# Performance work log

Measured on AMD Instinct MI355X. Metric: run time of the kernel, lower is better.

The kernel has to match this reference:

```python
import jax, jax.numpy as jnp
import numpy as np
from jax import lax

B, DEPTH, FS, C, NH = 4, 160, 4, 96, 4  # batch, temporal depth, feature_size, model_dims, heads
N = DEPTH * FS * FS                      # 2560 tokens
HD = C // NH                             # head dim 24
THETA = 0.6
BN_EPS = 1e-5
DN = ('NCDHW', 'OIDHW', 'NCDHW')


def setup_inputs() -> dict:
    key = jax.random.key(0)
    ks = jax.random.split(key, 16)
    x = jax.random.normal(ks[0], (B, N, C), jnp.float32)
    wq = jax.random.normal(ks[1], (C, C, 3, 3, 3), jnp.float32) * 0.02
    wk = jax.random.normal(ks[2], (C, C, 3, 3, 3), jnp.float32) * 0.02
    wv = jax.random.normal(ks[3], (C, C, 1, 1, 1), jnp.float32) * 0.1
    wo = jax.random.normal(ks[4], (C, C), jnp.float32) * 0.05
    bo = jnp.zeros((C,), jnp.float32)
    bnq_gamma = 1.0 + 0.1 * jax.random.normal(ks[5], (C,), jnp.float32)
    bnq_beta = 0.1 * jax.random.normal(ks[6], (C,), jnp.float32)
    bnq_mean = 0.1 * jax.random.normal(ks[7], (C,), jnp.float32)
    bnq_var = jax.random.uniform(ks[8], (C,), jnp.float32) + 0.5
    bnk_gamma = 1.0 + 0.1 * jax.random.normal(ks[9], (C,), jnp.float32)
    bnk_beta = 0.1 * jax.random.normal(ks[10], (C,), jnp.float32)
    bnk_mean = 0.1 * jax.random.normal(ks[11], (C,), jnp.float32)
    bnk_var = jax.random.uniform(ks[12], (C,), jnp.float32) + 0.5
    sharp_gradient = jnp.float32(np.sqrt(HD))
    return dict(x=x, sharp_gradient=sharp_gradient,
                wq=wq, bnq_gamma=bnq_gamma, bnq_beta=bnq_beta, bnq_mean=bnq_mean, bnq_var=bnq_var,
                wk=wk, bnk_gamma=bnk_gamma, bnk_beta=bnk_beta, bnk_mean=bnk_mean, bnk_var=bnk_var,
                wv=wv, wo=wo, bo=bo)


def _conv3d(x, w, pad):
    return lax.conv_general_dilated(x, w, (1, 1, 1), [(pad, pad)] * 3, dimension_numbers=DN)


def _tcdc(x, w):
    # normal conv + temporal center-difference correction
    out_normal = _conv3d(x, w, 1)
    kernel_diff = (w[:, :, 0].sum((-1, -2)) + w[:, :, -1].sum((-1, -2)))[:, :, None, None, None]
    out_diff = _conv3d(x, kernel_diff, 0)
    return out_normal - THETA * out_diff


def _bn(x, gamma, beta, mean, var):
    # eval-mode BatchNorm3d over channel axis 1
    sh = (1, -1, 1, 1, 1)
    scale = gamma.reshape(sh) * lax.rsqrt(var.reshape(sh) + BN_EPS)
    return (x - mean.reshape(sh)) * scale + beta.reshape(sh)


def _to_heads(t):
    # (B,C,D,H,W) -> (B,NH,N,HD)
    b = t.shape[0]
    t = t.reshape(b, C, N).transpose(0, 2, 1)          # (B,N,C)
    return t.reshape(b, N, NH, HD).transpose(0, 2, 1, 3)


def reference(x, sharp_gradient, wq, bnq_gamma, bnq_beta, bnq_mean, bnq_var,
              wk, bnk_gamma, bnk_beta, bnk_mean, bnk_var, wv, wo, bo):
    b = x.shape[0]
    xv = x.transpose(0, 2, 1).reshape(b, C, DEPTH, FS, FS)  # (B,C,D,H,W)
    q = _bn(_tcdc(xv, wq), bnq_gamma, bnq_beta, bnq_mean, bnq_var)
    k = _bn(_tcdc(xv, wk), bnk_gamma, bnk_beta, bnk_mean, bnk_var)
    v = _conv3d(xv, wv, 0)
    q, k, v = _to_heads(q), _to_heads(k), _to_heads(v)
    scores = jnp.einsum('bhnd,bhmd->bhnm', q, k) / sharp_gradient
    attn = jax.nn.softmax(scores, axis=-1)
    out = jnp.einsum('bhnm,bhmd->bhnd', attn, v)
    out = out.transpose(0, 2, 1, 3).reshape(b, N, C)   # merge heads
    return out @ wo.T + bo                              # out projection (dropout=eval)
```

## Files before the change

kernel.cpp:

```cpp
#include <hip/hip_runtime.h>
#include <hip/hip_bf16.h>

#define BB 4
#define DEPTH 160
#define CC 96
#define NN 2560
#define NHH 4
#define HD 24
#define THETA 0.6f
#define BN_EPS 1e-5f

typedef __attribute__((ext_vector_type(4))) float f32x4;
typedef __attribute__((ext_vector_type(8))) short s16x8;
typedef __attribute__((ext_vector_type(4))) short s16x4;
typedef __attribute__((ext_vector_type(2))) unsigned u32x2;
typedef __attribute__((ext_vector_type(4))) unsigned u32x4;

#if __has_builtin(__builtin_amdgcn_exp2f)
#define EXP2(x) __builtin_amdgcn_exp2f(x)
#else
#define EXP2(x) exp2f(x)
#endif

#define WS_WQ   0
#define WS_WK   124416
#define WS_WV   248832
#define WS_BQ   253440
#define WS_BK   253536
#define WS_ATT  253632
#define WS_QB   1236672
#define WS_KB   1892032
#define WS_VT   2547392
#define WS_WO   3202752

__device__ __forceinline__ short f2bf(float f) {
    unsigned u = __float_as_uint(f);
    u += 0x7fffu + ((u >> 16) & 1u);
    return (short)(u >> 16);
}
__device__ __forceinline__ unsigned bf16pk(float lo, float hi) {
    unsigned r;
    asm("v_cvt_pk_bf16_f32 %0, %1, %2" : "=v"(r) : "v"(lo), "v"(hi));
    return r;
}
__device__ __forceinline__ int vslot(int n) {
    return (n & 32) | (((n >> 2) & 3) << 3) | (((n >> 4) & 1) << 2) | (n & 3);
}

__global__ void prep_w(const float* __restrict__ w, const float* __restrict__ gamma,
                       const float* __restrict__ beta, const float* __restrict__ mean,
                       const float* __restrict__ var, short* __restrict__ w_eff,
                       float* __restrict__ bias,
                       const float* __restrict__ wv, short* __restrict__ wv_b) {
    int oc = blockIdx.x;
    int ic = threadIdx.x;
    if (ic >= CC) return;
    float scale = gamma[oc] * rsqrtf(var[oc] + BN_EPS);
    if (ic == 0) bias[oc] = beta[oc] - mean[oc] * scale;
    const float* wp = w + (oc * CC + ic) * 27;
    float kdiff = 0.f;
#pragma unroll
    for (int t = 0; t < 9; ++t) kdiff += wp[t] + wp[18 + t];
#pragma unroll
    for (int t = 0; t < 27; ++t) {
        float v = wp[t];
        if (t == 13) v -= THETA * kdiff;
        w_eff[t * (CC * CC) + oc * CC + ic] = f2bf(v * scale);
    }
    if (wv_b) wv_b[oc * CC + ic] = f2bf(wv[oc * CC + ic]);
}

__global__ void prep_wo(const float* __restrict__ wo, short* __restrict__ wo_b) {
    int i = blockIdx.x * 256 + threadIdx.x;
    if (i < CC * CC) {
        int oc = i / CC, ic = i % CC;
        wo_b[(((oc >> 4) * 3 + (ic >> 5)) << 9) + (oc & 15) * 32 + (ic & 31)] = f2bf(wo[i]);
    }
}

__global__ __launch_bounds__(192) void qkv_conv(
        const float* __restrict__ x, const short* __restrict__ wq_b,
        const short* __restrict__ wk_b, const short* __restrict__ wv_b,
        const float* __restrict__ bias_q, const float* __restrict__ bias_k,
        const float* __restrict__ sgp,
        short* __restrict__ Qb, short* __restrict__ Kb, short* __restrict__ Vtp) {
    __shared__ __align__(16) short xs[65 * 104];
    const int b = blockIdx.y;
    const int d0 = blockIdx.x * 2;
    const int z = blockIdx.z;
    const int tid = threadIdx.x;

#pragma unroll
    for (int k = 0; k < 8; ++k) {
        int c = tid + k * 192;
        int row = c / 24, ic0 = (c % 24) * 4;
        int dg = d0 - 1 + (row >> 4), pos = row & 15;
        u32x2 o = {0u, 0u};
        if (dg >= 0 && dg < DEPTH) {
            f32x4 v = *(const f32x4*)(x + ((size_t)(b * NN + dg * 16 + pos)) * CC + ic0);
            o[0] = bf16pk(v[0], v[1]);
            o[1] = bf16pk(v[2], v[3]);
        }
        *(u32x2*)&xs[row * 104 + ic0] = o;
    }
    if (tid < 26) *(u32x2*)&xs[64 * 104 + tid * 4] = (u32x2){0u, 0u};
    __syncthreads();

    const int w  = tid >> 6, l = tid & 63;
    const int j  = l & 15, g = l >> 4;
    const int oc0 = z * 48 + w * 16;
    const int hj = j >> 2, wj = j & 3;

    const short* wqlane = wq_b + (oc0 + j) * CC + 8 * g;
    const short* wklane = wk_b + (oc0 + j) * CC + 8 * g;
    const short* wvlane = wv_b + (oc0 + j) * CC + 8 * g;

    f32x4 accQA = {0,0,0,0}, accQB = {0,0,0,0};
    f32x4 accKA = {0,0,0,0}, accKB = {0,0,0,0};
    f32x4 avA   = {0,0,0,0}, avB   = {0,0,0,0};

    s16x8 wqc[3], wkc[3], wqn[3], wkn[3];
#pragma unroll
    for (int icb = 0; icb < 3; ++icb) {
        wqc[icb] = *(const s16x8*)(wqlane + icb * 32);
        wkc[icb] = *(const s16x8*)(wklane + icb * 32);
    }

#pragma unroll
    for (int tap = 0; tap < 27; ++tap) {
        if (tap < 26) {
#pragma unroll
            for (int icb = 0; icb < 3; ++icb) {
                wqn[icb] = *(const s16x8*)(wqlane + (tap + 1) * (CC * CC) + icb * 32);
                wkn[icb] = *(const s16x8*)(wklane + (tap + 1) * (CC * CC) + icb * 32);
            }
        }
        const int kd = tap / 9, kh = (tap / 3) % 3, kw = tap % 3;
        const int hh = hj + kh - 1, ww = wj + kw - 1;
        const bool valid = ((unsigned)hh < 4u) && ((unsigned)ww < 4u);
        const int rA = valid ? (kd * 16 + hh * 4 + ww) : 64;
        const int rB = valid ? ((1 + kd) * 16 + hh * 4 + ww) : 64;
        const short* xrA = &xs[rA * 104 + 8 * g];
        const short* xrB = &xs[rB * 104 + 8 * g];
#pragma unroll
        for (int icb = 0; icb < 3; ++icb) {
            s16x8 afA = *(const s16x8*)(xrA + icb * 32);
            s16x8 afB = *(const s16x8*)(xrB + icb * 32);
            accQA = __builtin_amdgcn_mfma_f32_16x16x32_bf16(afA, wqc[icb], accQA, 0, 0, 0);
            accQB = __builtin_amdgcn_mfma_f32_16x16x32_bf16(afB, wqc[icb], accQB, 0, 0, 0);
            accKA = __builtin_amdgcn_mfma_f32_16x16x32_bf16(afA, wkc[icb], accKA, 0, 0, 0);
            accKB = __builtin_amdgcn_mfma_f32_16x16x32_bf16(afB, wkc[icb], accKB, 0, 0, 0);
            if (tap == 13) {
                s16x8 bv = *(const s16x8*)(wvlane + icb * 32);
                avA = __builtin_amdgcn_mfma_f32_16x16x32_bf16(afA, bv, avA, 0, 0, 0);
                avB = __builtin_amdgcn_mfma_f32_16x16x32_bf16(afB, bv, avB, 0, 0, 0);
            }
        }
        if (tap < 26) {
#pragma unroll
            for (int icb = 0; icb < 3; ++icb) {
                wqc[icb] = wqn[icb];
                wkc[icb] = wkn[icb];
            }
        }
    }

    const float qs = 1.4426950408889634f / sgp[0];
    const int oc = oc0 + j, h = oc / HD, hd = oc % HD;
    const float bq_ = bias_q[oc], bk_ = bias_k[oc];
    const size_t headbase = (size_t)(b * NHH + h) * NN;
    short* QpA = Qb + (headbase + (d0 + 0) * 16 + 4 * g) * 32 + hd;
    short* QpB = Qb + (headbase + (d0 + 1) * 16 + 4 * g) * 32 + hd;
    short* KpA = Kb + (headbase + (d0 + 0) * 16 + 4 * g) * 32 + hd;
    short* KpB = Kb + (headbase + (d0 + 1) * 16 + 4 * g) * 32 + hd;
#pragma unroll
    for (int r = 0; r < 4; ++r) {
        QpA[r * 32] = f2bf((accQA[r] + bq_) * qs);
        QpB[r * 32] = f2bf((accQB[r] + bq_) * qs);
        KpA[r * 32] = f2bf(accKA[r] + bk_);
        KpB[r * 32] = f2bf(accKB[r] + bk_);
    }
    {
        short* Vb = Vtp + (size_t)(b * NHH + h) * (NN * 32);
        const int dh = hd >> 4, dj = hd & 15;
#pragma unroll
        for (int r = 0; r < 4; ++r) {
            int nA = d0 * 16 + 4 * g + r;
            int nB = nA + 16;
            int wA = vslot(nA & 63), wB = vslot(nB & 63);
            Vb[(nA >> 6) * 2048 + ((wA >> 5) * 2 + dh) * 512 + dj * 32 + (wA & 31)] = f2bf(avA[r]);
            Vb[(nB >> 6) * 2048 + ((wB >> 5) * 2 + dh) * 512 + dj * 32 + (wB & 31)] = f2bf(avB[r]);
        }
    }
    if (z == 0 && w == 0) {
        const int n = (d0 + ((l >> 4) & 1)) * 16 + (l & 15);
        const s16x8 z8 = {0, 0, 0, 0, 0, 0, 0, 0};
#pragma unroll
        for (int it = 0; it < 2; ++it) {
            int h2 = (l >> 5) + 2 * it;
            *(s16x8*)(Qb + ((size_t)(b * NHH + h2) * NN + n) * 32 + 24) = z8;
            *(s16x8*)(Kb + ((size_t)(b * NHH + h2) * NN + n) * 32 + 24) = z8;
        }
        const int wN = vslot(n & 63);
#pragma unroll
        for (int it2 = 0; it2 < 2; ++it2) {
            int h3 = it2 * 2 + (l >> 5);
            short* pb = Vtp + (size_t)(b * NHH + h3) * (NN * 32)
                      + (n >> 6) * 2048 + ((wN >> 5) * 2 + 1) * 512 + (wN & 31);
#pragma unroll
            for (int dj = 8; dj < 16; ++dj)
                pb[dj * 32] = 0;
        }
    }
}

#define SOFTTILE(S0, S1, S2, S3, MX, LP, OA, OB, P0, P1) {                      \
    float v0 = fmaxf(fmaxf(S0[0], S0[1]), fmaxf(S0[2], S0[3]));                 \
    float v1 = fmaxf(fmaxf(S1[0], S1[1]), fmaxf(S1[2], S1[3]));                 \
    float v2 = fmaxf(fmaxf(S2[0], S2[1]), fmaxf(S2[2], S2[3]));                 \
    float v3 = fmaxf(fmaxf(S3[0], S3[1]), fmaxf(S3[2], S3[3]));                 \
    float vmx = fmaxf(fmaxf(v0, v1), fmaxf(v2, v3));                            \
    vmx = fmaxf(vmx, __shfl_xor(vmx, 16));                                      \
    vmx = fmaxf(vmx, __shfl_xor(vmx, 32));                                      \
    float nm = fmaxf(MX, vmx);                                                  \
    float sc = EXP2(MX - nm);                                                   \
    MX = nm;                                                                    \
    LP *= sc; OA *= sc; OB *= sc;                                               \
    float p00 = EXP2(S0[0] - MX), p01 = EXP2(S0[1] - MX);                       \
    float p02 = EXP2(S0[2] - MX), p03 = EXP2(S0[3] - MX);                       \
    float p10 = EXP2(S1[0] - MX), p11 = EXP2(S1[1] - MX);                       \
    float p12 = EXP2(S1[2] - MX), p13 = EXP2(S1[3] - MX);                       \
    float p20 = EXP2(S2[0] - MX), p21 = EXP2(S2[1] - MX);                       \
    float p22 = EXP2(S2[2] - MX), p23 = EXP2(S2[3] - MX);                       \
    float p30 = EXP2(S3[0] - MX), p31 = EXP2(S3[1] - MX);                       \
    float p32 = EXP2(S3[2] - MX), p33 = EXP2(S3[3] - MX);                       \
    LP += (((p00 + p01) + (p02 + p03)) + ((p10 + p11) + (p12 + p13)))           \
        + (((p20 + p21) + (p22 + p23)) + ((p30 + p31) + (p32 + p33)));          \
    u32x4 w0_ = { bf16pk(p00, p01), bf16pk(p02, p03),                           \
                  bf16pk(p10, p11), bf16pk(p12, p13) };                         \
    u32x4 w1_ = { bf16pk(p20, p21), bf16pk(p22, p23),                           \
                  bf16pk(p30, p31), bf16pk(p32, p33) };                         \
    P0 = __builtin_bit_cast(s16x8, w0_);                                        \
    P1 = __builtin_bit_cast(s16x8, w1_);                                        \
}

__global__ __launch_bounds__(256) void attn_kernel(
        const short* __restrict__ Qb, const short* __restrict__ Kb,
        const short* __restrict__ Vtp, float* __restrict__ att) {
    __shared__ __align__(16) float comb[3][64][20];
    const int bh = blockIdx.x & 15;
    const int q0 = (blockIdx.x >> 4) * 32;
    const int b = bh >> 2, h = bh & 3;
    const int tid = threadIdx.x, wvid = tid >> 6, l = tid & 63;
    const int j = l & 15, g = l >> 4;

    const s16x8 qf0 = *(const s16x8*)(Qb + ((size_t)bh * NN + q0 + j) * 32 + 8 * g);
    const s16x8 qf1 = *(const s16x8*)(Qb + ((size_t)bh * NN + q0 + 16 + j) * 32 + 8 * g);
    const short* Kbase = Kb  + (size_t)bh * NN * 32 + (size_t)j * 32 + 8 * g;
    const short* Vbase = Vtp + (size_t)bh * NN * 32 + (size_t)j * 32 + 8 * g;

    f32x4 oA0 = {0,0,0,0}, oB0 = {0,0,0,0};
    f32x4 oA1 = {0,0,0,0}, oB1 = {0,0,0,0};
    float mx0 = -1e30f, lp0 = 0.f, mx1 = -1e30f, lp1 = 0.f;
    const f32x4 z = {0,0,0,0};

    const int tbeg = wvid * (NN / 4);
    const int tend = tbeg + NN / 4;

    for (int t0 = tbeg; t0 < tend; t0 += 64) {
        const short* kp = Kbase + (size_t)t0 * 32;
        s16x8 k0 = *(const s16x8*)(kp);
        s16x8 k1 = *(const s16x8*)(kp + 512);
        s16x8 k2 = *(const s16x8*)(kp + 1024);
        s16x8 k3 = *(const s16x8*)(kp + 1536);
        const short* vp = Vbase + (size_t)t0 * 32;
        s16x8 vA0 = *(const s16x8*)(vp);
        s16x8 vB0 = *(const s16x8*)(vp + 512);
        s16x8 vA1 = *(const s16x8*)(vp + 1024);
        s16x8 vB1 = *(const s16x8*)(vp + 1536);

        f32x4 s0 = __builtin_amdgcn_mfma_f32_16x16x32_bf16(k0, qf0, z, 0, 0, 0);
        f32x4 s1 = __builtin_amdgcn_mfma_f32_16x16x32_bf16(k1, qf0, z, 0, 0, 0);
        f32x4 s2 = __builtin_amdgcn_mfma_f32_16x16x32_bf16(k2, qf0, z, 0, 0, 0);
        f32x4 s3 = __builtin_amdgcn_mfma_f32_16x16x32_bf16(k3, qf0, z, 0, 0, 0);
        s16x8 P00, P01;
        SOFTTILE(s0, s1, s2, s3, mx0, lp0, oA0, oB0, P00, P01)

        f32x4 t0s = __builtin_amdgcn_mfma_f32_16x16x32_bf16(k0, qf1, z, 0, 0, 0);
        f32x4 t1s = __builtin_amdgcn_mfma_f32_16x16x32_bf16(k1, qf1, z, 0, 0, 0);
        f32x4 t2s = __builtin_amdgcn_mfma_f32_16x16x32_bf16(k2, qf1, z, 0, 0, 0);
        f32x4 t3s = __builtin_amdgcn_mfma_f32_16x16x32_bf16(k3, qf1, z, 0, 0, 0);
        s16x8 P10, P11;
        SOFTTILE(t0s, t1s, t2s, t3s, mx1, lp1, oA1, oB1, P10, P11)

        oA0 = __builtin_amdgcn_mfma_f32_16x16x32_bf16(vA0, P00, oA0, 0, 0, 0);
        oA0 = __builtin_amdgcn_mfma_f32_16x16x32_bf16(vA1, P01, oA0, 0, 0, 0);
        oB0 = __builtin_amdgcn_mfma_f32_16x16x32_bf16(vB0, P00, oB0, 0, 0, 0);
        oB0 = __builtin_amdgcn_mfma_f32_16x16x32_bf16(vB1, P01, oB0, 0, 0, 0);
        oA1 = __builtin_amdgcn_mfma_f32_16x16x32_bf16(vA0, P10, oA1, 0, 0, 0);
        oA1 = __builtin_amdgcn_mfma_f32_16x16x32_bf16(vA1, P11, oA1, 0, 0, 0);
        oB1 = __builtin_amdgcn_mfma_f32_16x16x32_bf16(vB0, P10, oB1, 0, 0, 0);
        oB1 = __builtin_amdgcn_mfma_f32_16x16x32_bf16(vB1, P11, oB1, 0, 0, 0);
    }

    lp0 += __shfl_xor(lp0, 16); lp0 += __shfl_xor(lp0, 32);
    lp1 += __shfl_xor(lp1, 16); lp1 += __shfl_xor(lp1, 32);

    if (wvid != 0) {
        float* cp = comb[wvid - 1][l];
        cp[0] = mx0; cp[1] = lp0; cp[2] = mx1; cp[3] = lp1;
        *(f32x4*)(cp + 4)  = oA0;
        *(f32x4*)(cp + 8)  = oB0;
        *(f32x4*)(cp + 12) = oA1;
        *(f32x4*)(cp + 16) = oB1;
    }
    __syncthreads();
    if (wvid != 0) return;

#pragma unroll
    for (int wv = 0; wv < 3; ++wv) {
        const float* cp = comb[wv][l];
        {
            float mb = cp[0], lb = cp[1];
            f32x4 oAb = *(const f32x4*)(cp + 4);
            f32x4 oBb = *(const f32x4*)(cp + 8);
            float mm = fmaxf(mx0, mb);
            float sa = EXP2(mx0 - mm), sb = EXP2(mb - mm);
            mx0 = mm;
            lp0 = lp0 * sa + lb * sb;
            oA0 = oA0 * sa + oAb * sb;
            oB0 = oB0 * sa + oBb * sb;
        }
        {
            float mb = cp[2], lb = cp[3];
            f32x4 oAb = *(const f32x4*)(cp + 12);
            f32x4 oBb = *(const f32x4*)(cp + 16);
            float mm = fmaxf(mx1, mb);
            float sa = EXP2(mx1 - mm), sb = EXP2(mb - mm);
            mx1 = mm;
            lp1 = lp1 * sa + lb * sb;
            oA1 = oA1 * sa + oAb * sb;
            oB1 = oB1 * sa + oBb * sb;
        }
    }

    const float rl0 = 1.f / lp0, rl1 = 1.f / lp1;
    f32x4 rA0 = oA0 * rl0, rB0 = oB0 * rl0;
    f32x4 rA1 = oA1 * rl1, rB1 = oB1 * rl1;

    float* op0 = att + ((size_t)b * NN + q0 + j) * CC + h * HD;
    float* op1 = att + ((size_t)b * NN + q0 + 16 + j) * CC + h * HD;
    *(f32x4*)(op0 + 4 * g) = rA0;
    *(f32x4*)(op1 + 4 * g) = rA1;
    if (g < 2) {
        *(f32x4*)(op0 + 16 + 4 * g) = rB0;
        *(f32x4*)(op1 + 16 + 4 * g) = rB1;
    }
}

__global__ __launch_bounds__(256) void proj_kernel(
        const float* __restrict__ att, const short* __restrict__ wo_b,
        const float* __restrict__ bo, float* __restrict__ out) {
    __shared__ __align__(16) short als[64 * 104];
    const int t0 = blockIdx.x * 64;
    const int tid = threadIdx.x;
#pragma unroll
    for (int k = 0; k < 6; ++k) {
        int c = tid + k * 256;
        int row = c / 24, ic0 = (c % 24) * 4;
        f32x4 v = *(const f32x4*)(att + (size_t)(t0 + row) * CC + ic0);
        u32x2 o = { bf16pk(v[0], v[1]), bf16pk(v[2], v[3]) };
        *(u32x2*)&als[row * 104 + ic0] = o;
    }
    __syncthreads();

    const int w = tid >> 6, l = tid & 63;
    const int j = l & 15, g = l >> 4;
    const short* ap = &als[(w * 16 + j) * 104 + 8 * g];
    s16x8 a0 = *(const s16x8*)(ap);
    s16x8 a1 = *(const s16x8*)(ap + 32);
    s16x8 a2 = *(const s16x8*)(ap + 64);
    const f32x4 zz = {0, 0, 0, 0};
    float* ob = out + (size_t)(t0 + w * 16 + 4 * g) * CC + j;
#pragma unroll
    for (int oct = 0; oct < 6; ++oct) {
        const short* wp = wo_b + oct * 3 * 512 + j * 32 + 8 * g;
        f32x4 acc = zz;
        acc = __builtin_amdgcn_mfma_f32_16x16x32_bf16(a0, *(const s16x8*)(wp),        acc, 0, 0, 0);
        acc = __builtin_amdgcn_mfma_f32_16x16x32_bf16(a1, *(const s16x8*)(wp + 512),  acc, 0, 0, 0);
        acc = __builtin_amdgcn_mfma_f32_16x16x32_bf16(a2, *(const s16x8*)(wp + 1024), acc, 0, 0, 0);
        const float bb = bo[oct * 16 + j];
#pragma unroll
        for (int r = 0; r < 4; ++r)
            ob[(size_t)r * CC + oct * 16] = acc[r] + bb;
    }
}

extern "C" void kernel_launch(void* const* d_in, const int* in_sizes, int n_in,
                              void* d_out, int out_size, void* d_ws, size_t ws_size,
                              hipStream_t stream) {
    const float* x     = (const float*)d_in[0];
    const float* sg    = (const float*)d_in[1];
    const float* wq    = (const float*)d_in[2];
    const float* bnq_g = (const float*)d_in[3];
    const float* bnq_b = (const float*)d_in[4];
    const float* bnq_m = (const float*)d_in[5];
    const float* bnq_v = (const float*)d_in[6];
    const float* wk    = (const float*)d_in[7];
    const float* bnk_g = (const float*)d_in[8];
    const float* bnk_b = (const float*)d_in[9];
    const float* bnk_m = (const float*)d_in[10];
    const float* bnk_v = (const float*)d_in[11];
    const float* wv    = (const float*)d_in[12];
    const float* wo    = (const float*)d_in[13];
    const float* bo    = (const float*)d_in[14];

    float* ws = (float*)d_ws;
    short* wq_b   = (short*)(ws + WS_WQ);
    short* wk_b   = (short*)(ws + WS_WK);
    short* wv_b   = (short*)(ws + WS_WV);
    float* bias_q = ws + WS_BQ;
    float* bias_k = ws + WS_BK;
    float* attw   = ws + WS_ATT;
    short* Qb     = (short*)(ws + WS_QB);
    short* Kb     = (short*)(ws + WS_KB);
    short* Vtp    = (short*)(ws + WS_VT);
    short* wo_b   = (short*)(ws + WS_WO);

    prep_w<<<dim3(CC), dim3(128), 0, stream>>>(wq, bnq_g, bnq_b, bnq_m, bnq_v, wq_b, bias_q,
                                               wv, wv_b);
    prep_w<<<dim3(CC), dim3(128), 0, stream>>>(wk, bnk_g, bnk_b, bnk_m, bnk_v, wk_b, bias_k,
                                               nullptr, nullptr);
    prep_wo<<<dim3(36), dim3(256), 0, stream>>>(wo, wo_b);

    qkv_conv<<<dim3(DEPTH / 2, BB, 2), dim3(192), 0, stream>>>(
        x, wq_b, wk_b, wv_b, bias_q, bias_k, sg, Qb, Kb, Vtp);

    attn_kernel<<<dim3(NN / 32 * 16), dim3(256), 0, stream>>>(Qb, Kb, Vtp, attw);

    proj_kernel<<<dim3(BB * NN / 64), dim3(256), 0, stream>>>(attw, wo_b, bo, (float*)d_out);
}
```

Baseline: 78.48 us.

## Stage conv weights through LDS in two-tap groups with fragment-major layout

The Q/K weight prep now writes weights in a fragment-major layout indexed by tap, output-channel half, 16-oc tile and 32-ic block. The conv kernel loads two taps of Q and K weights cooperatively into shared memory per group and reads MFMA B-fragments from LDS, replacing per-lane global loads with register double-buffering. This gives coalesced 16-byte global loads and shares weights across the three waves. In exchange it adds about 36 KB of LDS per block, two barriers per group and a non-unrolled outer loop, which may cut occupancy and serialize load and compute.

```diff
diff --git a/kernel.cpp b/kernel.cpp
--- a/kernel.cpp
+++ b/kernel.cpp
@@ -61,11 +61,14 @@
     float kdiff = 0.f;
 #pragma unroll
     for (int t = 0; t < 9; ++t) kdiff += wp[t] + wp[18 + t];
+    const int zh = oc / 48, oct = (oc % 48) >> 4, jj = oc & 15;
+    const int icb = ic >> 5, icw = ic & 31;
+    const int fo = oct * 3 + icb;
 #pragma unroll
     for (int t = 0; t < 27; ++t) {
         float v = wp[t];
         if (t == 13) v -= THETA * kdiff;
-        w_eff[t * (CC * CC) + oc * CC + ic] = f2bf(v * scale);
+        w_eff[(size_t)((t * 2 + zh) * 9 + fo) * 512 + jj * 32 + icw] = f2bf(v * scale);
     }
     if (wv_b) wv_b[oc * CC + ic] = f2bf(wv[oc * CC + ic]);
 }
@@ -85,6 +88,7 @@
         const float* __restrict__ sgp,
         short* __restrict__ Qb, short* __restrict__ Kb, short* __restrict__ Vtp) {
     __shared__ __align__(16) short xs[65 * 104];
+    __shared__ __align__(16) short wl[4 * 4608];
     const int b = blockIdx.y;
     const int d0 = blockIdx.x * 2;
     const int z = blockIdx.z;
@@ -104,63 +108,85 @@
         *(u32x2*)&xs[row * 104 + ic0] = o;
     }
     if (tid < 26) *(u32x2*)&xs[64 * 104 + tid * 4] = (u32x2){0u, 0u};
-    __syncthreads();
 
     const int w  = tid >> 6, l = tid & 63;
     const int j  = l & 15, g = l >> 4;
     const int oc0 = z * 48 + w * 16;
     const int hj = j >> 2, wj = j & 3;
-
-    const short* wqlane = wq_b + (oc0 + j) * CC + 8 * g;
-    const short* wklane = wk_b + (oc0 + j) * CC + 8 * g;
+    const int lof = j * 32 + 8 * g;
+
     const short* wvlane = wv_b + (oc0 + j) * CC + 8 * g;
+    s16x8 bv0 = *(const s16x8*)(wvlane);
+    s16x8 bv1 = *(const s16x8*)(wvlane + 32);
+    s16x8 bv2 = *(const s16x8*)(wvlane + 64);
 
     f32x4 accQA = {0,0,0,0}, accQB = {0,0,0,0};
     f32x4 accKA = {0,0,0,0}, accKB = {0,0,0,0};
     f32x4 avA   = {0,0,0,0}, avB   = {0,0,0,0};
 
-    s16x8 wqc[3], wkc[3], wqn[3], wkn[3];
-#pragma unroll
-    for (int icb = 0; icb < 3; ++icb) {
-        wqc[icb] = *(const s16x8*)(wqlane + icb * 32);
-        wkc[icb] = *(const s16x8*)(wklane + icb * 32);
-    }
-
-#pragma unroll
-    for (int tap = 0; tap < 27; ++tap) {
-        if (tap < 26) {
+    __syncthreads();
+
+#pragma unroll 1
+    for (int grp = 0; grp < 14; ++grp) {
+        const int g0 = grp * 2;
+        const int two = (g0 < 26) ? 1 : 0;
+        const int nchunk = two ? 12 : 6;
+        const int perarr = two ? 1152 : 576;
+        s16x8 tmp[12];
+        int dsts[12];
+#pragma unroll
+        for (int i = 0; i < 12; ++i) {
+            if (i < nchunk) {
+                int idx = tid + i * 192;
+                int arr = (idx >= perarr) ? 1 : 0;
+                int ridx = idx - arr * perarr;
+                int tp = (ridx >= 576) ? 1 : 0;
+                int rem = (ridx - tp * 576) * 8;
+                const short* gsrc = (arr ? wk_b : wq_b)
+                    + (size_t)((g0 + tp) * 2 + z) * 4608 + rem;
+                tmp[i] = *(const s16x8*)gsrc;
+                dsts[i] = (arr * 2 + tp) * 4608 + rem;
+            }
+        }
+        __syncthreads();
+#pragma unroll
+        for (int i = 0; i < 12; ++i)
+            if (i < nchunk) *(s16x8*)&wl[dsts[i]] = tmp[i];
+        __syncthreads();
+
+#pragma unroll
+        for (int tp = 0; tp < 2; ++tp) {
+            const int tap = g0 + tp;
+            if (tap > 26) break;
+            const int kd = tap / 9, kh = (tap / 3) % 3, kw = tap % 3;
+            const int hh = hj + kh - 1, ww = wj + kw - 1;
+            const bool valid = ((unsigned)hh < 4u) && ((unsigned)ww < 4u);
+            const int rA = valid ? (kd * 16 + hh * 4 + ww) : 64;
+            const int rB = valid ? ((1 + kd) * 16 + hh * 4 + ww) : 64;
+            const short* xrA = &xs[rA * 104 + 8 * g];
+            const short* xrB = &xs[rB * 104 + 8 * g];
+            const short* wqf = &wl[tp * 4608 + (w * 3) * 512 + lof];
+            const short* wkf = &wl[(2 + tp) * 4608 + (w * 3) * 512 + lof];
 #pragma unroll
             for (int icb = 0; icb < 3; ++icb) {
-                wqn[icb] = *(const s16x8*)(wqlane + (tap + 1) * (CC * CC) + icb * 32);
-                wkn[icb] = *(const s16x8*)(wklane + (tap + 1) * (CC * CC) + icb * 32);
+                s16x8 afA = *(const s16x8*)(xrA + icb * 32);
+                s16x8 afB = *(const s16x8*)(xrB + icb * 32);
+                s16x8 bq  = *(const s16x8*)(wqf + icb * 512);
+                s16x8 bk  = *(const s16x8*)(wkf + icb * 512);
+                accQA = __builtin_amdgcn_mfma_f32_16x16x32_bf16(afA, bq, accQA, 0, 0, 0);
+                accQB = __builtin_amdgcn_mfma_f32_16x16x32_bf16(afB, bq, accQB, 0, 0, 0);
+                accKA = __builtin_amdgcn_mfma_f32_16x16x32_bf16(afA, bk, accKA, 0, 0, 0);
+                accKB = __builtin_amdgcn_mfma_f32_16x16x32_bf16(afB, bk, accKB, 0, 0, 0);
             }
-        }
-        const int kd = tap / 9, kh = (tap / 3) % 3, kw = tap % 3;
-        const int hh = hj + kh - 1, ww = wj + kw - 1;
-        const bool valid = ((unsigned)hh < 4u) && ((unsigned)ww < 4u);
-        const int rA = valid ? (kd * 16 + hh * 4 + ww) : 64;
-        const int rB = valid ? ((1 + kd) * 16 + hh * 4 + ww) : 64;
-        const short* xrA = &xs[rA * 104 + 8 * g];
-        const short* xrB = &xs[rB * 104 + 8 * g];
-#pragma unroll
-        for (int icb = 0; icb < 3; ++icb) {
-            s16x8 afA = *(const s16x8*)(xrA + icb * 32);
-            s16x8 afB = *(const s16x8*)(xrB + icb * 32);
-            accQA = __builtin_amdgcn_mfma_f32_16x16x32_bf16(afA, wqc[icb], accQA, 0, 0, 0);
-            accQB = __builtin_amdgcn_mfma_f32_16x16x32_bf16(afB, wqc[icb], accQB, 0, 0, 0);
-            accKA = __builtin_amdgcn_mfma_f32_16x16x32_bf16(afA, wkc[icb], accKA, 0, 0, 0);
-            accKB = __builtin_amdgcn_mfma_f32_16x16x32_bf16(afB, wkc[icb], accKB, 0, 0, 0);
             if (tap == 13) {
-                s16x8 bv = *(const s16x8*)(wvlane + icb * 32);
-                avA = __builtin_amdgcn_mfma_f32_16x16x32_bf16(afA, bv, avA, 0, 0, 0);
-                avB = __builtin_amdgcn_mfma_f32_16x16x32_bf16(afB, bv, avB, 0, 0, 0);
-            }
-        }
-        if (tap < 26) {
-#pragma unroll
-            for (int icb = 0; icb < 3; ++icb) {
-                wqc[icb] = wqn[icb];
-                wkc[icb] = wkn[icb];
+#pragma unroll
+                for (int icb = 0; icb < 3; ++icb) {
+                    s16x8 afA = *(const s16x8*)(xrA + icb * 32);
+                    s16x8 afB = *(const s16x8*)(xrB + icb * 32);
+                    s16x8 bb = (icb == 0) ? bv0 : (icb == 1) ? bv1 : bv2;
+                    avA = __builtin_amdgcn_mfma_f32_16x16x32_bf16(afA, bb, avA, 0, 0, 0);
+                    avB = __builtin_amdgcn_mfma_f32_16x16x32_bf16(afB, bb, avB, 0, 0, 0);
+                }
             }
         }
     }
```

Result: slower. 84.12 us (+7.2%).

## Split qkv conv taps across two wave halves with LDS reduction

Applied to the files above, without the earlier changes.

The qkv_conv block doubles to 384 threads. Each output-channel tile's 27 conv taps are split between two waves (taps 0-13 and 14-26), and the second wave's partial Q/K accumulators are combined through shared memory before the epilogue. This shortens the serial MFMA chain per wave and doubles the waves per block to improve latency hiding. The cost is extra LDS, a second barrier, and idle waves during the epilogue.

```diff
diff --git a/kernel.cpp b/kernel.cpp
--- a/kernel.cpp
+++ b/kernel.cpp
@@ -78,21 +78,77 @@
     }
 }
 
-__global__ __launch_bounds__(192) void qkv_conv(
+#define MFMA16(A, B, C) __builtin_amdgcn_mfma_f32_16x16x32_bf16(A, B, C, 0, 0, 0)
+
+template<int TB, int TE>
+__device__ __forceinline__ void conv_taps(
+        const short* __restrict__ wqlane, const short* __restrict__ wklane,
+        const short* __restrict__ wvlane, const short* xs,
+        int hj, int wj, int g,
+        f32x4& accQA, f32x4& accQB, f32x4& accKA, f32x4& accKB,
+        f32x4& avA, f32x4& avB) {
+    s16x8 wqc[3], wkc[3], wqn[3], wkn[3];
+#pragma unroll
+    for (int icb = 0; icb < 3; ++icb) {
+        wqc[icb] = *(const s16x8*)(wqlane + TB * (CC * CC) + icb * 32);
+        wkc[icb] = *(const s16x8*)(wklane + TB * (CC * CC) + icb * 32);
+    }
+#pragma unroll
+    for (int tap = TB; tap < TE; ++tap) {
+        if (tap < TE - 1) {
+#pragma unroll
+            for (int icb = 0; icb < 3; ++icb) {
+                wqn[icb] = *(const s16x8*)(wqlane + (tap + 1) * (CC * CC) + icb * 32);
+                wkn[icb] = *(const s16x8*)(wklane + (tap + 1) * (CC * CC) + icb * 32);
+            }
+        }
+        const int kd = tap / 9, kh = (tap / 3) % 3, kw = tap % 3;
+        const int hh = hj + kh - 1, ww = wj + kw - 1;
+        const bool valid = ((unsigned)hh < 4u) && ((unsigned)ww < 4u);
+        const int rA = valid ? (kd * 16 + hh * 4 + ww) : 64;
+        const int rB = valid ? ((1 + kd) * 16 + hh * 4 + ww) : 64;
+        const short* xrA = &xs[rA * 104 + 8 * g];
+        const short* xrB = &xs[rB * 104 + 8 * g];
+#pragma unroll
+        for (int icb = 0; icb < 3; ++icb) {
+            s16x8 afA = *(const s16x8*)(xrA + icb * 32);
+            s16x8 afB = *(const s16x8*)(xrB + icb * 32);
+            accQA = MFMA16(afA, wqc[icb], accQA);
+            accQB = MFMA16(afB, wqc[icb], accQB);
+            accKA = MFMA16(afA, wkc[icb], accKA);
+            accKB = MFMA16(afB, wkc[icb], accKB);
+            if (tap == 13) {
+                s16x8 bv = *(const s16x8*)(wvlane + icb * 32);
+                avA = MFMA16(afA, bv, avA);
+                avB = MFMA16(afB, bv, avB);
+            }
+        }
+        if (tap < TE - 1) {
+#pragma unroll
+            for (int icb = 0; icb < 3; ++icb) {
+                wqc[icb] = wqn[icb];
+                wkc[icb] = wkn[icb];
+            }
+        }
+    }
+}
+
+__global__ __launch_bounds__(384) void qkv_conv(
         const float* __restrict__ x, const short* __restrict__ wq_b,
         const short* __restrict__ wk_b, const short* __restrict__ wv_b,
         const float* __restrict__ bias_q, const float* __restrict__ bias_k,
         const float* __restrict__ sgp,
         short* __restrict__ Qb, short* __restrict__ Kb, short* __restrict__ Vtp) {
     __shared__ __align__(16) short xs[65 * 104];
+    __shared__ __align__(16) float comb[3][64][16];
     const int b = blockIdx.y;
     const int d0 = blockIdx.x * 2;
     const int z = blockIdx.z;
     const int tid = threadIdx.x;
 
 #pragma unroll
-    for (int k = 0; k < 8; ++k) {
-        int c = tid + k * 192;
+    for (int k = 0; k < 4; ++k) {
+        int c = tid + k * 384;
         int row = c / 24, ic0 = (c % 24) * 4;
         int dg = d0 - 1 + (row >> 4), pos = row & 15;
         u32x2 o = {0u, 0u};
@@ -106,9 +162,10 @@
     if (tid < 26) *(u32x2*)&xs[64 * 104 + tid * 4] = (u32x2){0u, 0u};
     __syncthreads();
 
-    const int w  = tid >> 6, l = tid & 63;
-    const int j  = l & 15, g = l >> 4;
-    const int oc0 = z * 48 + w * 16;
+    const int w = tid >> 6, l = tid & 63;
+    const int oct = w % 3, half = w / 3;
+    const int j = l & 15, g = l >> 4;
+    const int oc0 = z * 48 + oct * 16;
     const int hj = j >> 2, wj = j & 3;
 
     const short* wqlane = wq_b + (oc0 + j) * CC + 8 * g;
@@ -119,50 +176,28 @@
     f32x4 accKA = {0,0,0,0}, accKB = {0,0,0,0};
     f32x4 avA   = {0,0,0,0}, avB   = {0,0,0,0};
 
-    s16x8 wqc[3], wkc[3], wqn[3], wkn[3];
-#pragma unroll
-    for (int icb = 0; icb < 3; ++icb) {
-        wqc[icb] = *(const s16x8*)(wqlane + icb * 32);
-        wkc[icb] = *(const s16x8*)(wklane + icb * 32);
-    }
-
-#pragma unroll
-    for (int tap = 0; tap < 27; ++tap) {
-        if (tap < 26) {
-#pragma unroll
-            for (int icb = 0; icb < 3; ++icb) {
-                wqn[icb] = *(const s16x8*)(wqlane + (tap + 1) * (CC * CC) + icb * 32);
-                wkn[icb] = *(const s16x8*)(wklane + (tap + 1) * (CC * CC) + icb * 32);
-            }
-        }
-        const int kd = tap / 9, kh = (tap / 3) % 3, kw = tap % 3;
-        const int hh = hj + kh - 1, ww = wj + kw - 1;
-        const bool valid = ((unsigned)hh < 4u) && ((unsigned)ww < 4u);
-        const int rA = valid ? (kd * 16 + hh * 4 + ww) : 64;
-        const int rB = valid ? ((1 + kd) * 16 + hh * 4 + ww) : 64;
-        const short* xrA = &xs[rA * 104 + 8 * g];
-        const short* xrB = &xs[rB * 104 + 8 * g];
-#pragma unroll
-        for (int icb = 0; icb < 3; ++icb) {
-            s16x8 afA = *(const s16x8*)(xrA + icb * 32);
-            s16x8 afB = *(const s16x8*)(xrB + icb * 32);
-            accQA = __builtin_amdgcn_mfma_f32_16x16x32_bf16(afA, wqc[icb], accQA, 0, 0, 0);
-            accQB = __builtin_amdgcn_mfma_f32_16x16x32_bf16(afB, wqc[icb], accQB, 0, 0, 0);
-            accKA = __builtin_amdgcn_mfma_f32_16x16x32_bf16(afA, wkc[icb], accKA, 0, 0, 0);
-            accKB = __builtin_amdgcn_mfma_f32_16x16x32_bf16(afB, wkc[icb], accKB, 0, 0, 0);
-            if (tap == 13) {
-                s16x8 bv = *(const s16x8*)(wvlane + icb * 32);
-                avA = __builtin_amdgcn_mfma_f32_16x16x32_bf16(afA, bv, avA, 0, 0, 0);
-                avB = __builtin_amdgcn_mfma_f32_16x16x32_bf16(afB, bv, avB, 0, 0, 0);
-            }
-        }
-        if (tap < 26) {
-#pragma unroll
-            for (int icb = 0; icb < 3; ++icb) {
-                wqc[icb] = wqn[icb];
-                wkc[icb] = wkn[icb];
-            }
-        }
+    if (half == 0)
+        conv_taps<0, 14>(wqlane, wklane, wvlane, xs, hj, wj, g,
+                         accQA, accQB, accKA, accKB, avA, avB);
+    else
+        conv_taps<14, 27>(wqlane, wklane, wvlane, xs, hj, wj, g,
+                          accQA, accQB, accKA, accKB, avA, avB);
+
+    if (half == 1) {
+        float* cp = comb[oct][l];
+        *(f32x4*)(cp)      = accQA;
+        *(f32x4*)(cp + 4)  = accQB;
+        *(f32x4*)(cp + 8)  = accKA;
+        *(f32x4*)(cp + 12) = accKB;
+    }
+    __syncthreads();
+    if (half != 0) return;
+    {
+        const float* cp = comb[oct][l];
+        accQA += *(const f32x4*)(cp);
+        accQB += *(const f32x4*)(cp + 4);
+        accKA += *(const f32x4*)(cp + 8);
+        accKB += *(const f32x4*)(cp + 12);
     }
 
     const float qs = 1.4426950408889634f / sgp[0];
@@ -192,7 +227,7 @@
             Vb[(nB >> 6) * 2048 + ((wB >> 5) * 2 + dh) * 512 + dj * 32 + (wB & 31)] = f2bf(avB[r]);
         }
     }
-    if (z == 0 && w == 0) {
+    if (z == 0 && oct == 0) {
         const int n = (d0 + ((l >> 4) & 1)) * 16 + (l & 15);
         const s16x8 z8 = {0, 0, 0, 0, 0, 0, 0, 0};
 #pragma unroll
@@ -433,7 +468,7 @@
                                                nullptr, nullptr);
     prep_wo<<<dim3(36), dim3(256), 0, stream>>>(wo, wo_b);
 
-    qkv_conv<<<dim3(DEPTH / 2, BB, 2), dim3(192), 0, stream>>>(
+    qkv_conv<<<dim3(DEPTH / 2, BB, 2), dim3(384), 0, stream>>>(
         x, wq_b, wk_b, wv_b, bias_q, bias_k, sg, Qb, Kb, Vtp);
 
     attn_kernel<<<dim3(NN / 32 * 16), dim3(256), 0, stream>>>(Qb, Kb, Vtp, attw);
```

Result: slower. 93.80 us (+19.5%).
